# Performance work log

Hardware: AMD Instinct MI355X
Metric: run time of the kernel (lower is better)

Reference implementation:

```python
import jax, jax.numpy as jnp
import numpy as np


def setup_inputs() -> dict:
    key = jax.random.key(0)
    k1, k2, k3, k4, k5, k6 = jax.random.split(key, 6)
    b, L, h, eh, M, N = 16, 256, 256, 64, 128, 128
    X = jax.random.normal(k1, (b, L, h), dtype=jnp.float32)
    E = jax.random.normal(k2, (b, L, L, eh), dtype=jnp.float32)
    A = jax.random.uniform(k3, (b, L, L), dtype=jnp.float32)
    w = jax.random.normal(k4, (b, L, 1), dtype=jnp.float32)
    mask = jnp.ones((b, L, L), dtype=bool)
    mol_lens = jax.random.randint(k5, (b, 2), 64, M + 1, dtype=jnp.int32)
    # force one row to the max so M,N match torch.max(mol_lens) exactly
    mol_lens = mol_lens.at[0].set(jnp.array([M, N], dtype=jnp.int32))
    return {"X": X, "E": E, "A": A, "w": w, "mask": mask,
            "mol_lens": mol_lens, "M": M, "N": N}


def reference(X, E, A, w, mask, mol_lens, M, N):
    b, L, h = X.shape
    eh = E.shape[-1]
    l0 = mol_lens[:, 0][:, None]            # [b,1]
    l1 = mol_lens[:, 1][:, None]
    p1 = jnp.arange(2 * M)[None, :]         # [1,2M]
    p2 = jnp.arange(2 * N)[None, :]         # [1,2N]

    # duplicate-and-pad source indices (note: X2 copies X[:, :l1], per source)
    src1 = jnp.clip(jnp.where(p1 < l0, p1, p1 - l0), 0, L - 1)          # [b,2M]
    srcX2 = jnp.clip(jnp.where(p2 < l1, p2, p2 - l1), 0, L - 1)         # [b,2N]
    srcE2 = jnp.clip(l0 + jnp.where(p2 < l1, p2, p2 - l1), 0, L - 1)    # [b,2N]
    valid1 = p1 < 2 * l0                    # [b,2M]
    valid2 = p2 < 2 * l1                    # [b,2N]

    bi = jnp.arange(b)[:, None]
    X1 = jnp.where(valid1[..., None], X[bi, src1], 0.0)                 # [b,2M,h]
    X2 = jnp.where(valid2[..., None], X[bi, srcX2], 0.0)                # [b,2N,h]

    # block-diagonal validity: (first copy x first copy) | (second x second)
    f1 = p1 < l0
    s1 = (p1 >= l0) & valid1
    blk1 = (f1[:, :, None] & f1[:, None, :]) | (s1[:, :, None] & s1[:, None, :])
    f2 = p2 < l1
    s2 = (p2 >= l1) & valid2
    blk2 = (f2[:, :, None] & f2[:, None, :]) | (s2[:, :, None] & s2[:, None, :])

    bii = jnp.arange(b)[:, None, None]
    g1 = E[bii, src1[:, :, None], src1[:, None, :]]                     # [b,2M,2M,eh]
    E1 = jnp.where(blk1[..., None], g1, 0.0)
    A1 = jnp.where(blk1, A[bii, src1[:, :, None], src1[:, None, :]], 0.0)
    g2 = E[bii, srcE2[:, :, None], srcE2[:, None, :]]                   # [b,2N,2N,eh]
    E2 = jnp.where(blk2[..., None], g2, 0.0)
    A2 = jnp.where(blk2, A[bii, srcE2[:, :, None], srcE2[:, None, :]], 0.0)

    w1 = jnp.zeros((b, 2 * M, 1), X.dtype)
    w2 = jnp.zeros((b, 2 * N, 1), X.dtype)

    # cross-copy masks on padded tensors
    mask1 = ~((f1[:, :, None] & s1[:, None, :]) | (s1[:, :, None] & f1[:, None, :]))
    mask2 = ~((f2[:, :, None] & s2[:, None, :]) | (s2[:, :, None] & f2[:, None, :]))

    # in-place edits of input mask: True on [:l0,:l0] and [l0:,l0:], False on cross
    q = jnp.arange(L)[None, :]
    lsum = l0 + l1
    left = q < l0                           # [b,L]
    midd = (q >= l0) & (q < lsum)
    cond_true = (left[:, :, None] & left[:, None, :]) | ((~left)[:, :, None] & (~left)[:, None, :])
    cond_false = (left[:, :, None] & midd[:, None, :]) | (midd[:, :, None] & left[:, None, :])
    mask_out = jnp.where(cond_true, True, jnp.where(cond_false, False, mask))

    return (X1, X2, E1, E2, A1, A2, mask1, mask2, w1, w2, mask_out)
```

## Files before the change

### kernel.cpp

```cpp
#include <hip/hip_runtime.h>


#define OFF_X1   0
#define OFF_X2   1048576
#define OFF_E1   2097152
#define OFF_E2   69206016
#define OFF_A1   136314880
#define OFF_A2   137363456
#define OFF_M1   138412032
#define OFF_M2   139460608
#define OFF_W1   140509184
#define OFF_MO   140517376

__global__ __launch_bounds__(256) void e_gather_kernel(
    const float4* __restrict__ E,
    const int* __restrict__ mol_lens,
    float4* __restrict__ out,
    int lenIdx, int useOffset)
{
    int t = blockIdx.x * 256 + threadIdx.x;
    int c = t & 15;
    int q = (t >> 4) & 255;
    int p = (t >> 12) & 255;
    int i = t >> 20;

    int l    = mol_lens[i * 2 + lenIdx];
    int base = useOffset ? mol_lens[i * 2] : 0;

    bool fp = p < l;
    bool sp = (!fp) && (p < 2 * l);
    bool fq = q < l;
    bool sq = (!fq) && (q < 2 * l);

    float4 v = make_float4(0.f, 0.f, 0.f, 0.f);
    if ((fp && fq) || (sp && sq)) {
        int ip = base + (fp ? p : p - l); if (ip > 255) ip = 255;
        int iq = base + (fq ? q : q - l); if (iq > 255) iq = 255;
        v = E[((i * 256 + ip) * 256 + iq) * 16 + c];
    }
    out[t] = v;
}

__global__ __launch_bounds__(256) void small_kernel(
    const float* __restrict__ X,
    const float* __restrict__ A,
    const int* __restrict__ mask,
    const int* __restrict__ mol_lens,
    float* __restrict__ out)
{
    int t = blockIdx.x * 256 + threadIdx.x;
    int q = t & 255;
    int p = (t >> 8) & 255;
    int i = t >> 16;

    int l0 = mol_lens[i * 2];
    int l1 = mol_lens[i * 2 + 1];

    bool v1 = p < 2 * l0;
    int  s1p = (p < l0) ? p : p - l0;
    out[OFF_X1 + t] = v1 ? X[(i * 256 + s1p) * 256 + q] : 0.f;

    bool v2 = p < 2 * l1;
    int  s2p = (p < l1) ? p : p - l1;
    out[OFF_X2 + t] = v2 ? X[(i * 256 + s2p) * 256 + q] : 0.f;

    bool f1p = p < l0, s1pb = (!f1p) && v1;
    bool f1q = q < l0, s1qb = (!f1q) && (q < 2 * l0);
    int  s1q = f1q ? q : q - l0;
    bool blk1 = (f1p && f1q) || (s1pb && s1qb);
    out[OFF_A1 + t] = blk1 ? A[(i * 256 + s1p) * 256 + s1q] : 0.f;
    out[OFF_M1 + t] = ((f1p && s1qb) || (s1pb && f1q)) ? 0.f : 1.f;

    bool f2p = p < l1, s2pb = (!f2p) && v2;
    bool f2q = q < l1, s2qb = (!f2q) && (q < 2 * l1);
    int  e2p = l0 + (f2p ? p : p - l1); if (e2p > 255) e2p = 255;
    int  e2q = l0 + (f2q ? q : q - l1); if (e2q > 255) e2q = 255;
    bool blk2 = (f2p && f2q) || (s2pb && s2qb);
    out[OFF_A2 + t] = blk2 ? A[(i * 256 + e2p) * 256 + e2q] : 0.f;
    out[OFF_M2 + t] = ((f2p && s2qb) || (s2pb && f2q)) ? 0.f : 1.f;

    bool leftp = p < l0, leftq = q < l0;
    int  lsum = l0 + l1;
    bool middp = (!leftp) && (p < lsum);
    bool middq = (!leftq) && (q < lsum);
    bool ct = (leftp && leftq) || ((!leftp) && (!leftq));
    bool cf = (leftp && middq) || (middp && leftq);
    float mv;
    if (ct)      mv = 1.f;
    else if (cf) mv = 0.f;
    else         mv = (mask[t] != 0) ? 1.f : 0.f;
    out[OFF_MO + t] = mv;

    if (t < 8192) out[OFF_W1 + t] = 0.f;
}

extern "C" void kernel_launch(void* const* d_in, const int* in_sizes, int n_in,
                              void* d_out, int out_size, void* d_ws, size_t ws_size,
                              hipStream_t stream) {
    const float* X        = (const float*)d_in[0];
    const float* E        = (const float*)d_in[1];
    const float* A        = (const float*)d_in[2];
    const int*   mask     = (const int*)d_in[4];
    const int*   mol_lens = (const int*)d_in[5];

    float* out = (float*)d_out;

    e_gather_kernel<<<65536, 256, 0, stream>>>(
        (const float4*)E, mol_lens, (float4*)(out + OFF_E1), 0, 0);
    e_gather_kernel<<<65536, 256, 0, stream>>>(
        (const float4*)E, mol_lens, (float4*)(out + OFF_E2), 1, 1);
    small_kernel<<<4096, 256, 0, stream>>>(X, A, mask, mol_lens, out);
}
```

Baseline: 711.6 us.

## Fuse E1/E2 gathers and small outputs into one kernel with nontemporal stores

Replaces three launches with a single kernel. Each thread writes its slot of both E1 and E2, and the first 4096 blocks also produce the X/A/mask outputs. All stores become nontemporal so the roughly 540 MB of streaming output does not pollute the caches. The change removes launch gaps and lets the E1 and E2 gathers share reads of E, at the cost of higher per-thread work and some block imbalance.

```diff
diff --git a/kernel.cpp b/kernel.cpp
--- a/kernel.cpp
+++ b/kernel.cpp
@@ -12,86 +12,110 @@
 #define OFF_W1   140509184
 #define OFF_MO   140517376
 
-__global__ __launch_bounds__(256) void e_gather_kernel(
-    const float4* __restrict__ E,
-    const int* __restrict__ mol_lens,
-    float4* __restrict__ out,
-    int lenIdx, int useOffset)
-{
-    int t = blockIdx.x * 256 + threadIdx.x;
-    int c = t & 15;
-    int q = (t >> 4) & 255;
-    int p = (t >> 12) & 255;
-    int i = t >> 20;
+#define OFF_E1_V4 (OFF_E1 / 4)
+#define OFF_E2_V4 (OFF_E2 / 4)
 
-    int l    = mol_lens[i * 2 + lenIdx];
-    int base = useOffset ? mol_lens[i * 2] : 0;
+typedef float f32x4 __attribute__((ext_vector_type(4)));
 
-    bool fp = p < l;
-    bool sp = (!fp) && (p < 2 * l);
-    bool fq = q < l;
-    bool sq = (!fq) && (q < 2 * l);
-
-    float4 v = make_float4(0.f, 0.f, 0.f, 0.f);
-    if ((fp && fq) || (sp && sq)) {
-        int ip = base + (fp ? p : p - l); if (ip > 255) ip = 255;
-        int iq = base + (fq ? q : q - l); if (iq > 255) iq = 255;
-        v = E[((i * 256 + ip) * 256 + iq) * 16 + c];
-    }
-    out[t] = v;
-}
-
-__global__ __launch_bounds__(256) void small_kernel(
+__global__ __launch_bounds__(256) void fused_kernel(
+    const f32x4* __restrict__ E,
     const float* __restrict__ X,
     const float* __restrict__ A,
-    const int* __restrict__ mask,
-    const int* __restrict__ mol_lens,
-    float* __restrict__ out)
+    const int*   __restrict__ mask,
+    const int*   __restrict__ mol_lens,
+    float*       __restrict__ out)
 {
-    int t = blockIdx.x * 256 + threadIdx.x;
-    int q = t & 255;
-    int p = (t >> 8) & 255;
-    int i = t >> 16;
+    const int bb  = blockIdx.x;
+    const int tid = threadIdx.x;
 
-    int l0 = mol_lens[i * 2];
-    int l1 = mol_lens[i * 2 + 1];
+    const int i = bb >> 12;
+    const int p = (bb >> 4) & 255;
+    const int q = ((bb & 15) << 4) | (tid >> 4);
+    const int c = tid & 15;
+    const int t = bb * 256 + tid;
 
-    bool v1 = p < 2 * l0;
-    int  s1p = (p < l0) ? p : p - l0;
-    out[OFF_X1 + t] = v1 ? X[(i * 256 + s1p) * 256 + q] : 0.f;
+    const int l0 = mol_lens[i * 2];
+    const int l1 = mol_lens[i * 2 + 1];
 
-    bool v2 = p < 2 * l1;
-    int  s2p = (p < l1) ? p : p - l1;
-    out[OFF_X2 + t] = v2 ? X[(i * 256 + s2p) * 256 + q] : 0.f;
+    f32x4* outv4 = (f32x4*)out;
 
-    bool f1p = p < l0, s1pb = (!f1p) && v1;
-    bool f1q = q < l0, s1qb = (!f1q) && (q < 2 * l0);
-    int  s1q = f1q ? q : q - l0;
-    bool blk1 = (f1p && f1q) || (s1pb && s1qb);
-    out[OFF_A1 + t] = blk1 ? A[(i * 256 + s1p) * 256 + s1q] : 0.f;
-    out[OFF_M1 + t] = ((f1p && s1qb) || (s1pb && f1q)) ? 0.f : 1.f;
+    {
+        const bool fp = p < l0, sp = !fp && (p < 2 * l0);
+        const bool fq = q < l0, sq = !fq && (q < 2 * l0);
+        f32x4 v = (f32x4)(0.f, 0.f, 0.f, 0.f);
+        if ((fp && fq) || (sp && sq)) {
+            const int ip = fp ? p : p - l0;
+            const int iq = fq ? q : q - l0;
+            v = E[((i * 256 + ip) * 256 + iq) * 16 + c];
+        }
+        __builtin_nontemporal_store(v, &outv4[OFF_E1_V4 + t]);
+    }
 
-    bool f2p = p < l1, s2pb = (!f2p) && v2;
-    bool f2q = q < l1, s2qb = (!f2q) && (q < 2 * l1);
-    int  e2p = l0 + (f2p ? p : p - l1); if (e2p > 255) e2p = 255;
-    int  e2q = l0 + (f2q ? q : q - l1); if (e2q > 255) e2q = 255;
-    bool blk2 = (f2p && f2q) || (s2pb && s2qb);
-    out[OFF_A2 + t] = blk2 ? A[(i * 256 + e2p) * 256 + e2q] : 0.f;
-    out[OFF_M2 + t] = ((f2p && s2qb) || (s2pb && f2q)) ? 0.f : 1.f;
+    {
+        const bool fp = p < l1, sp = !fp && (p < 2 * l1);
+        const bool fq = q < l1, sq = !fq && (q < 2 * l1);
+        f32x4 v = (f32x4)(0.f, 0.f, 0.f, 0.f);
+        if ((fp && fq) || (sp && sq)) {
+            int ip = l0 + (fp ? p : p - l1); if (ip > 255) ip = 255;
+            int iq = l0 + (fq ? q : q - l1); if (iq > 255) iq = 255;
+            v = E[((i * 256 + ip) * 256 + iq) * 16 + c];
+        }
+        __builtin_nontemporal_store(v, &outv4[OFF_E2_V4 + t]);
+    }
 
-    bool leftp = p < l0, leftq = q < l0;
-    int  lsum = l0 + l1;
-    bool middp = (!leftp) && (p < lsum);
-    bool middq = (!leftq) && (q < lsum);
-    bool ct = (leftp && leftq) || ((!leftp) && (!leftq));
-    bool cf = (leftp && middq) || (middp && leftq);
-    float mv;
-    if (ct)      mv = 1.f;
-    else if (cf) mv = 0.f;
-    else         mv = (mask[t] != 0) ? 1.f : 0.f;
-    out[OFF_MO + t] = mv;
+    if (bb < 4096) {
+        const int ts = t;
+        const int qs = tid;
+        const int ps = bb & 255;
+        const int is = bb >> 8;
 
-    if (t < 8192) out[OFF_W1 + t] = 0.f;
+        const int sl0 = mol_lens[is * 2];
+        const int sl1 = mol_lens[is * 2 + 1];
+
+        const bool v1  = ps < 2 * sl0;
+        const int  s1p = (ps < sl0) ? ps : ps - sl0;
+        __builtin_nontemporal_store(
+            v1 ? X[(is * 256 + s1p) * 256 + qs] : 0.f, &out[OFF_X1 + ts]);
+
+        const bool v2  = ps < 2 * sl1;
+        const int  s2p = (ps < sl1) ? ps : ps - sl1;
+        __builtin_nontemporal_store(
+            v2 ? X[(is * 256 + s2p) * 256 + qs] : 0.f, &out[OFF_X2 + ts]);
+
+        const bool f1p = ps < sl0, s1pb = (!f1p) && v1;
+        const bool f1q = qs < sl0, s1qb = (!f1q) && (qs < 2 * sl0);
+        const int  s1q = f1q ? qs : qs - sl0;
+        const bool blk1 = (f1p && f1q) || (s1pb && s1qb);
+        __builtin_nontemporal_store(
+            blk1 ? A[(is * 256 + s1p) * 256 + s1q] : 0.f, &out[OFF_A1 + ts]);
+        __builtin_nontemporal_store(
+            ((f1p && s1qb) || (s1pb && f1q)) ? 0.f : 1.f, &out[OFF_M1 + ts]);
+
+        const bool f2p = ps < sl1, s2pb = (!f2p) && v2;
+        const bool f2q = qs < sl1, s2qb = (!f2q) && (qs < 2 * sl1);
+        int e2p = sl0 + (f2p ? ps : ps - sl1); if (e2p > 255) e2p = 255;
+        int e2q = sl0 + (f2q ? qs : qs - sl1); if (e2q > 255) e2q = 255;
+        const bool blk2 = (f2p && f2q) || (s2pb && s2qb);
+        __builtin_nontemporal_store(
+            blk2 ? A[(is * 256 + e2p) * 256 + e2q] : 0.f, &out[OFF_A2 + ts]);
+        __builtin_nontemporal_store(
+            ((f2p && s2qb) || (s2pb && f2q)) ? 0.f : 1.f, &out[OFF_M2 + ts]);
+
+        const bool leftp = ps < sl0, leftq = qs < sl0;
+        const int  lsum  = sl0 + sl1;
+        const bool middp = (!leftp) && (ps < lsum);
+        const bool middq = (!leftq) && (qs < lsum);
+        const bool ct = (leftp && leftq) || ((!leftp) && (!leftq));
+        const bool cf = (leftp && middq) || (middp && leftq);
+        float mv;
+        if (ct)      mv = 1.f;
+        else if (cf) mv = 0.f;
+        else         mv = (mask[ts] != 0) ? 1.f : 0.f;
+        __builtin_nontemporal_store(mv, &out[OFF_MO + ts]);
+
+        if (ts < 8192)
+            __builtin_nontemporal_store(0.f, &out[OFF_W1 + ts]);
+    }
 }
 
 extern "C" void kernel_launch(void* const* d_in, const int* in_sizes, int n_in,
@@ -105,9 +129,6 @@
 
     float* out = (float*)d_out;
 
-    e_gather_kernel<<<65536, 256, 0, stream>>>(
-        (const float4*)E, mol_lens, (float4*)(out + OFF_E1), 0, 0);
-    e_gather_kernel<<<65536, 256, 0, stream>>>(
-        (const float4*)E, mol_lens, (float4*)(out + OFF_E2), 1, 1);
-    small_kernel<<<4096, 256, 0, stream>>>(X, A, mask, mol_lens, out);
+    fused_kernel<<<65536, 256, 0, stream>>>(
+        (const f32x4*)E, X, A, mask, mol_lens, out);
 }
```

Result: faster. 694.5 us (-2.4%).
